# Kernel tuning notes

Measured on AMD Instinct MI355X. Metric: run time of the kernel, lower is better.

The kernel has to match this reference:

```python
import jax, jax.numpy as jnp
import numpy as np

# dims derived from init_kwargs
B, C, T, F = 16, 2, 16, 256
TP, FP = 4, 4            # time/freq patch
MF = F // FP             # 64 freq tokens
TIC = T // TP            # 4 time tokens per chunk
S = MF * TIC             # 256 tokens per chunk
CTX = 3
LEFT = S * CTX           # 768 cached tokens
MT = TIC * (CTX + 1)     # 16 max time positions
D, H, G = 512, 8, 4      # d_model, q heads, kv groups
HD = D // H              # 64
R = H // G               # 2 q-heads per kv group
L = 4                    # layers
FFH = 4 * D
EPS = 1e-5


def _ln(x, g, b):
    m = jnp.mean(x, -1, keepdims=True)
    v = jnp.mean((x - m) ** 2, -1, keepdims=True)
    return (x - m) * jax.lax.rsqrt(v + EPS) * g + b


def setup_inputs() -> dict:
    key = jax.random.key(0)
    ks = iter(jax.random.split(key, 20))
    rn = lambda shape, s=0.05: jax.random.normal(next(ks), shape, jnp.float32) * s
    return {
        "x": rn((B, C, T, F), 1.0),
        "cache_k": rn((L, B, G, LEFT, HD), 1.0),
        "cache_v": rn((L, B, G, LEFT, HD), 1.0),
        "in_W": rn((TP * FP * C, D)), "in_b": jnp.zeros((D,)),
        "ln1_g": jnp.ones((L, D)), "ln1_b": jnp.zeros((L, D)),
        "Wq": rn((L, D, D)), "bq": jnp.zeros((L, D)),
        "Wk": rn((L, D, G * HD)), "bk": jnp.zeros((L, G * HD)),
        "Wv": rn((L, D, G * HD)), "bv": jnp.zeros((L, G * HD)),
        "Wo": rn((L, D, D)), "bo": jnp.zeros((L, D)),
        "rel_time": rn((L, 2 * MT - 1, H)), "rel_freq": rn((L, 2 * MF - 1, H)),
        "res_a": jnp.ones((L,)),
        "ln2_g": jnp.ones((L, D)), "ln2_b": jnp.zeros((L, D)),
        "W1": rn((L, D, FFH)), "b1": jnp.zeros((L, FFH)),
        "W3": rn((L, D, FFH)), "b3": jnp.zeros((L, FFH)),
        "W2": rn((L, FFH, D)), "b2": jnp.zeros((L, D)),
        "res_f": jnp.ones((L,)),
        "out_W": rn((D, TP * FP * C)), "out_b": jnp.zeros((TP * FP * C,)),
    }


def reference(x, cache_k, cache_v, in_W, in_b, ln1_g, ln1_b, Wq, bq, Wk, bk, Wv, bv,
              Wo, bo, rel_time, rel_freq, res_a, ln2_g, ln2_b, W1, b1, W3, b3, W2, b2,
              res_f, out_W, out_b):
    # patchify: (B,C,T,F) -> (B, S, TP*FP*C), token order time-major / freq inner
    h = jnp.transpose(x, (0, 2, 3, 1)).reshape(B, TIC, TP, MF, FP, C)
    h = jnp.transpose(h, (0, 1, 3, 2, 4, 5)).reshape(B, S, TP * FP * C)
    h = h @ in_W + in_b  # (B,S,D)

    # 2D relative position indices (identical each layer)
    K = LEFT + S
    q_idx = jnp.arange(S)
    k_idx = jnp.arange(K)
    qt = LEFT // MF + q_idx // MF  # query time = cache time offset + local time
    qf = q_idx % MF
    kt = k_idx // MF
    kf = k_idx % MF
    dt = qt[:, None] - kt[None, :] + (MT - 1)  # (S,K) in [0, 2*MT-2]
    df = qf[:, None] - kf[None, :] + (MF - 1)  # (S,K) in [0, 2*MF-2]
    scale = 1.0 / np.sqrt(HD).astype(np.float32)

    new_ck, new_cv = [], []
    for l in range(L):
        # --- streaming GQA attention with 2D rel-pos and KV cache ---
        xin = _ln(h, ln1_g[l], ln1_b[l])
        q = (xin @ Wq[l] + bq[l]).reshape(B, S, H, HD)
        k = (xin @ Wk[l] + bk[l]).reshape(B, S, G, HD)
        v = (xin @ Wv[l] + bv[l]).reshape(B, S, G, HD)
        k_full = jnp.concatenate([cache_k[l], jnp.transpose(k, (0, 2, 1, 3))], axis=2)  # (B,G,K,HD)
        v_full = jnp.concatenate([cache_v[l], jnp.transpose(v, (0, 2, 1, 3))], axis=2)
        new_ck.append(k_full[:, :, -LEFT:])
        new_cv.append(v_full[:, :, -LEFT:])
        # group q heads: head h -> group h // R
        scores = jnp.einsum('bsgrd,bgtd->bgrst', q.reshape(B, S, G, R, HD), k_full) * scale
        bias = rel_time[l][dt] + rel_freq[l][df]          # (S,K,H)
        bias = jnp.transpose(bias, (2, 0, 1)).reshape(G, R, S, K)
        attn = jax.nn.softmax(scores + bias[None], axis=-1)
        o = jnp.einsum('bgrst,bgtd->bsgrd', attn, v_full).reshape(B, S, D)
        o = o @ Wo[l] + bo[l]
        h = h + res_a[l] * o  # dropout/droppath identity at eval
        # --- SwiGLU FFN ---
        xin = _ln(h, ln2_g[l], ln2_b[l])
        ff = (jax.nn.silu(xin @ W1[l] + b1[l]) * (xin @ W3[l] + b3[l])) @ W2[l] + b2[l]
        h = h + res_f[l] * ff

    y = h @ out_W + out_b  # (B,S,TP*FP*C)
    # unpatchify back to (B,C,T,F)
    y = y.reshape(B, TIC, MF, TP, FP, C)
    y = jnp.transpose(y, (0, 1, 3, 2, 4, 5)).reshape(B, T, F, C)
    y = jnp.transpose(y, (0, 3, 1, 2))
    return y, jnp.stack(new_ck), jnp.stack(new_cv)
```

## Files before the change

kernel.cpp:

```cpp
#include <hip/hip_runtime.h>
#include <stdint.h>

typedef __attribute__((ext_vector_type(8))) short bf16x8;
typedef __attribute__((ext_vector_type(4))) float f32x4;

#define B_    16
#define S_    256
#define LEFT_ 768
#define KT_   1024
#define D_    512
#define H_    8
#define G_    4
#define HD_   64
#define L_    4
#define FFH_  2048
#define M_    4096

__device__ __forceinline__ unsigned short f2b(float f){
  unsigned u = __float_as_uint(f);
  u += 0x7fffu + ((u>>16)&1u);
  return (unsigned short)(u>>16);
}

__device__ __forceinline__ void gl_lds16(const unsigned short* g, void* l){
  __builtin_amdgcn_global_load_lds(
    (const __attribute__((address_space(1))) unsigned int*)g,
    (__attribute__((address_space(3))) unsigned int*)l, 16, 0, 0);
}

template<int BM, int BN, int WM, int WN, class BRowF>
__device__ __forceinline__ void mfma_core(
    const unsigned short* Abase, int lda, int m0, BRowF brow,
    int kd, char* As, char* Bs, f32x4* acc)
{
  constexpr int FR = WM/16, FC = WN/16;
  constexpr int NWC = BN/WN;
  constexpr int CA = BM/64, CB = BN/64;
  const int tid = threadIdx.x, wave = tid>>6, lane = tid&63;
  const int wr = wave / NWC, wc = wave % NWC;
  const int lr = lane>>2;
  const int swl = (lane&3) ^ ((lane>>2)&3) ^ (lane>>4);

  auto stage = [&](int buf, int k0){
    #pragma unroll
    for (int i = 0; i < CA; ++i) {
      const int chunk = wave*CA + i;
      const unsigned short* gp = Abase + (size_t)(m0 + chunk*16 + lr)*lda + k0 + swl*8;
      gl_lds16(gp, As + buf*(BM*64) + chunk*1024);
    }
    #pragma unroll
    for (int i = 0; i < CB; ++i) {
      const int chunk = wave*CB + i;
      const unsigned short* gp = brow(chunk*16 + lr) + k0 + swl*8;
      gl_lds16(gp, Bs + buf*(BN*64) + chunk*1024);
    }
  };

  stage(0, 0);
  __syncthreads();
  int cur = 0;
  for (int k0 = 0; k0 < kd; k0 += 32) {
    if (k0 + 32 < kd) stage(cur^1, k0 + 32);
    bf16x8 af[FR], bfr[FC];
    #pragma unroll
    for (int r = 0; r < FR; ++r)
      af[r] = *(const bf16x8*)(As + cur*(BM*64) + (wr*WM + r*16 + (lane&15))*64 + swl*16);
    #pragma unroll
    for (int c = 0; c < FC; ++c)
      bfr[c] = *(const bf16x8*)(Bs + cur*(BN*64) + (wc*WN + c*16 + (lane&15))*64 + swl*16);
    #pragma unroll
    for (int r = 0; r < FR; ++r)
      #pragma unroll
      for (int c = 0; c < FC; ++c)
        acc[r*FC+c] = __builtin_amdgcn_mfma_f32_16x16x32_bf16(af[r], bfr[c], acc[r*FC+c], 0, 0, 0);
    __syncthreads();
    cur ^= 1;
  }
}

__global__ __launch_bounds__(256) void transpose_cvt(
    const float* __restrict__ src, unsigned short* __restrict__ dst,
    int K, int N, int ntk, int ntn)
{
  __shared__ float t[64][65];
  int bx = blockIdx.x;
  int kt = bx % ntk; int nt = (bx/ntk) % ntn; int l = bx/(ntk*ntn);
  src += (size_t)l*K*N; dst += (size_t)l*N*K;
  const int k0 = kt*64, n0 = nt*64;
  const int tid = threadIdx.x;
  #pragma unroll
  for (int i = 0; i < 4; ++i) {
    int kr = (tid>>4) + i*16;
    const float4 v = *(const float4*)&src[(size_t)(k0+kr)*N + n0 + (tid&15)*4];
    t[kr][(tid&15)*4+0]=v.x; t[kr][(tid&15)*4+1]=v.y;
    t[kr][(tid&15)*4+2]=v.z; t[kr][(tid&15)*4+3]=v.w;
  }
  __syncthreads();
  const int nn = tid>>2, kk = (tid&3)*16;
  unsigned w[8];
  #pragma unroll
  for (int j = 0; j < 8; ++j)
    w[j] = (unsigned)f2b(t[kk+2*j][nn]) | ((unsigned)f2b(t[kk+2*j+1][nn])<<16);
  size_t off = (size_t)(n0+nn)*K + k0 + kk;
  *(uint4*)&dst[off]     = make_uint4(w[0],w[1],w[2],w[3]);
  *(uint4*)&dst[off + 8] = make_uint4(w[4],w[5],w[6],w[7]);
}

__global__ __launch_bounds__(256) void patchify_inproj(
    const float* __restrict__ x, const float* __restrict__ inW,
    const float* __restrict__ inb, float* __restrict__ h)
{
  int bs = blockIdx.x;
  int b = bs >> 8, s = bs & 255;
  int tic = s >> 6, mf = s & 63;
  __shared__ float ps[32];
  int tid = threadIdx.x;
  if (tid < 32) {
    int tp = tid >> 3, fp = (tid >> 1) & 3, c = tid & 1;
    ps[tid] = x[((size_t)(b*2 + c)*16 + tic*4 + tp)*256 + mf*4 + fp];
  }
  __syncthreads();
  #pragma unroll
  for (int rep = 0; rep < 2; ++rep) {
    int d = tid + rep*256;
    float acc = inb[d];
    #pragma unroll
    for (int i = 0; i < 32; ++i) acc += ps[i] * inW[i*D_ + d];
    h[(size_t)bs*D_ + d] = acc;
  }
}

__global__ __launch_bounds__(256) void ln_kernel(
    const float* __restrict__ in, unsigned short* __restrict__ out,
    const float* __restrict__ g, const float* __restrict__ bta)
{
  size_t row = blockIdx.x;
  const float* rp = in + row*D_;
  int tid = threadIdx.x;
  float x0 = rp[tid], x1 = rp[tid+256];
  float s = x0 + x1, sq = x0*x0 + x1*x1;
  __shared__ float red[10];
  #pragma unroll
  for (int o = 32; o > 0; o >>= 1) {
    s  += __shfl_down(s,  o, 64);
    sq += __shfl_down(sq, o, 64);
  }
  if ((tid & 63) == 0) { red[tid>>6] = s; red[4 + (tid>>6)] = sq; }
  __syncthreads();
  if (tid == 0) {
    float ts = red[0]+red[1]+red[2]+red[3];
    float tq = red[4]+red[5]+red[6]+red[7];
    float mean = ts * (1.0f/D_);
    float var  = tq * (1.0f/D_) - mean*mean;
    red[8] = mean; red[9] = 1.0f / sqrtf(var + 1e-5f);
  }
  __syncthreads();
  float mean = red[8], inv = red[9];
  unsigned short* op = out + row*D_;
  op[tid]     = f2b((x0-mean)*inv*g[tid]     + bta[tid]);
  op[tid+256] = f2b((x1-mean)*inv*g[tid+256] + bta[tid+256]);
}

__global__ __launch_bounds__(256) void qkv_gemm(
    const unsigned short* __restrict__ xin,
    const unsigned short* __restrict__ Wqt, const unsigned short* __restrict__ Wkt,
    const unsigned short* __restrict__ Wvt,
    const float* __restrict__ bq, const float* __restrict__ bk_, const float* __restrict__ bv_,
    unsigned short* __restrict__ q_bf, unsigned short* __restrict__ kf_bf,
    unsigned short* __restrict__ vt_bf, float* __restrict__ nck, float* __restrict__ ncv)
{
  __shared__ alignas(16) char As[2*128*64];
  __shared__ alignas(16) char Bs[2*128*64];
  f32x4 acc[16] = {};
  const int bx = blockIdx.x;
  const int mt = bx >> 3, nt = bx & 7;
  const int m0 = mt*128, n0 = nt*128;
  auto brow = [&](int r) -> const unsigned short* {
    int n = n0 + r;
    return n < 512 ? Wqt + (size_t)n*512
         : n < 768 ? Wkt + (size_t)(n-512)*512
                   : Wvt + (size_t)(n-768)*512;
  };
  mfma_core<128,128,64,64>(xin, 512, m0, brow, 512, As, Bs, acc);
  const int lane = threadIdx.x & 63, wave = threadIdx.x >> 6;
  const int wr = wave >> 1, wc = wave & 1;
  #pragma unroll
  for (int r = 0; r < 4; ++r)
  #pragma unroll
  for (int c = 0; c < 4; ++c) {
    f32x4 v = acc[r*4+c];
    #pragma unroll
    for (int reg = 0; reg < 4; ++reg) {
      int m = m0 + wr*64 + r*16 + ((lane>>4)<<2) + reg;
      int n = n0 + wc*64 + c*16 + (lane&15);
      float val = v[reg];
      int b = m >> 8, s = m & 255;
      if (n < 512) {
        q_bf[(size_t)m*512 + n] = f2b(val + bq[n]);
      } else if (n < 768) {
        int g = (n-512) >> 6, hd = n & 63;
        float kv = val + bk_[n-512];
        kf_bf[((size_t)(b*4+g)*1024 + 768 + s)*64 + hd] = f2b(kv);
        nck [((size_t)(b*4+g)*768  + 512 + s)*64 + hd] = kv;
      } else {
        int g = (n-768) >> 6, hd = n & 63;
        float vv = val + bv_[n-768];
        vt_bf[((size_t)(b*4+g)*64 + hd)*1024 + 768 + s] = f2b(vv);
        ncv  [((size_t)(b*4+g)*768 + 512 + s)*64 + hd] = vv;
      }
    }
  }
}

__global__ __launch_bounds__(256) void merge_k(
    const float* __restrict__ ck, unsigned short* __restrict__ kf_bf,
    float* __restrict__ nck)
{
  size_t idx = (size_t)blockIdx.x*256 + threadIdx.x;
  int hd4 = idx & 15;
  size_t t  = (idx >> 4) % 768;
  size_t bg = idx / (16*768);
  const float4 v = ((const float4*)ck)[idx];
  uint2 pk;
  pk.x = (unsigned)f2b(v.x) | ((unsigned)f2b(v.y)<<16);
  pk.y = (unsigned)f2b(v.z) | ((unsigned)f2b(v.w)<<16);
  *(uint2*)&kf_bf[((bg*1024 + t)*64) + hd4*4] = pk;
  if (t >= 256)
    ((float4*)nck)[(bg*768 + (t-256))*16 + hd4] = v;
}

__global__ __launch_bounds__(256) void merge_vt(
    const float* __restrict__ cv, unsigned short* __restrict__ vt_bf,
    float* __restrict__ ncv)
{
  __shared__ float t[64][65];
  const int bg = blockIdx.x / 12, tt = blockIdx.x % 12;
  const int t0 = tt*64;
  const int tid = threadIdx.x;
  #pragma unroll
  for (int i = 0; i < 4; ++i) {
    int tr = (tid>>4) + i*16;
    const float4 v = ((const float4*)cv)[((size_t)bg*768 + t0+tr)*16 + (tid&15)];
    t[tr][(tid&15)*4+0]=v.x; t[tr][(tid&15)*4+1]=v.y;
    t[tr][(tid&15)*4+2]=v.z; t[tr][(tid&15)*4+3]=v.w;
    if (t0+tr >= 256)
      ((float4*)ncv)[((size_t)bg*768 + t0+tr-256)*16 + (tid&15)] = v;
  }
  __syncthreads();
  const int hd = tid>>2, tc = (tid&3)*16;
  unsigned w[8];
  #pragma unroll
  for (int j = 0; j < 8; ++j)
    w[j] = (unsigned)f2b(t[tc+2*j][hd]) | ((unsigned)f2b(t[tc+2*j+1][hd])<<16);
  size_t off = ((size_t)bg*64 + hd)*1024 + t0 + tc;
  *(uint4*)&vt_bf[off]     = make_uint4(w[0],w[1],w[2],w[3]);
  *(uint4*)&vt_bf[off + 8] = make_uint4(w[4],w[5],w[6],w[7]);
}

__global__ __launch_bounds__(256) void flash_attn(
    const unsigned short* __restrict__ q_bf,
    const unsigned short* __restrict__ kf_bf,
    const unsigned short* __restrict__ vt_bf,
    const float* __restrict__ relt,
    const float* __restrict__ relf,
    unsigned short* __restrict__ att_bf)
{
  const int bx = blockIdx.x;
  const int qt = bx & 3, hh = (bx>>2) & 7, b = bx >> 5;
  const int g = hh >> 1;
  const int tid = threadIdx.x, wave = tid>>6, lane = tid&63;
  const int lg = lane>>4, lq = lane&15;
  const int q0 = qt*64;

  __shared__ alignas(16) char Ks[2][8192];
  __shared__ alignas(16) char Vs[2][8192];

  const unsigned short* kfb  = kf_bf + (size_t)(b*4+g)*1024*64;
  const unsigned short* vtb2 = vt_bf + (size_t)(b*4+g)*64*1024;

  auto stage = [&](int buf, int t){
    #pragma unroll
    for (int it = 0; it < 2; ++it) {
      int slot = it*256 + tid;
      int r = slot>>3, p = slot&7, u = p ^ (r&7);
      gl_lds16(kfb + (size_t)(t*64 + r)*64 + u*8, Ks[buf] + slot*16);
      gl_lds16(vtb2 + (size_t)r*1024 + t*64 + u*8, Vs[buf] + slot*16);
    }
  };

  const unsigned short* qrow = q_bf + ((size_t)(b*256 + q0 + wave*16 + lq))*512 + hh*64;
  bf16x8 qfrag[2];
  qfrag[0] = *(const bf16x8*)(qrow + lg*8);
  qfrag[1] = *(const bf16x8*)(qrow + 32 + lg*8);

  float bias_f[4][4];
  {
    int sq = wave*16 + lq;
    #pragma unroll
    for (int f = 0; f < 4; ++f)
      #pragma unroll
      for (int r = 0; r < 4; ++r)
        bias_f[f][r] = relf[((sq - (f*16 + lg*4 + r)) + 63)*8 + hh];
  }

  f32x4 ot[4] = {};
  float m_run = -1e30f, l_part = 0.f;

  stage(0, 0);
  __syncthreads();

  for (int t = 0; t < 16; ++t) {
    const int cur = t & 1;
    if (t + 1 < 16) stage(cur^1, t+1);

    f32x4 st[4] = {};
    #pragma unroll
    for (int c = 0; c < 2; ++c)
      #pragma unroll
      for (int f = 0; f < 4; ++f) {
        int row = f*16 + lq;
        int pu = (c*4 + lg) ^ (row & 7);
        bf16x8 kf_ = *(const bf16x8*)(Ks[cur] + row*128 + pu*16);
        st[f] = __builtin_amdgcn_mfma_f32_16x16x32_bf16(kf_, qfrag[c], st[f], 0,0,0);
      }

    const float bias_t = relt[(27 + qt - t)*8 + hh];
    float mt = -1e30f;
    #pragma unroll
    for (int f = 0; f < 4; ++f)
      #pragma unroll
      for (int r = 0; r < 4; ++r) {
        float v = st[f][r]*0.125f + bias_t + bias_f[f][r];
        st[f][r] = v;
        mt = fmaxf(mt, v);
      }
    mt = fmaxf(mt, __shfl_xor(mt, 16, 64));
    mt = fmaxf(mt, __shfl_xor(mt, 32, 64));
    const float m_new = fmaxf(m_run, mt);
    const float corr = __expf(m_run - m_new);
    m_run = m_new;
    l_part *= corr;
    #pragma unroll
    for (int f = 0; f < 4; ++f) {
      ot[f][0] *= corr; ot[f][1] *= corr; ot[f][2] *= corr; ot[f][3] *= corr;
    }
    float psum = 0.f;
    unsigned r01[4], r23[4];
    #pragma unroll
    for (int f = 0; f < 4; ++f) {
      float e0 = __expf(st[f][0] - m_new);
      float e1 = __expf(st[f][1] - m_new);
      float e2 = __expf(st[f][2] - m_new);
      float e3 = __expf(st[f][3] - m_new);
      psum += (e0+e1)+(e2+e3);
      r01[f] = (unsigned)f2b(e0) | ((unsigned)f2b(e1)<<16);
      r23[f] = (unsigned)f2b(e2) | ((unsigned)f2b(e3)<<16);
    }
    l_part += psum;

    const int src0 = (lg&1)*32 + lq;
    const int src1 = src0 + 16;
    const bool hi = (lg>>1) != 0;
    #pragma unroll
    for (int c = 0; c < 2; ++c) {
      unsigned a0 = (unsigned)__shfl((int)r01[c*2],   src0, 64);
      unsigned b0 = (unsigned)__shfl((int)r01[c*2+1], src0, 64);
      unsigned a1 = (unsigned)__shfl((int)r23[c*2],   src0, 64);
      unsigned b1 = (unsigned)__shfl((int)r23[c*2+1], src0, 64);
      unsigned a2 = (unsigned)__shfl((int)r01[c*2],   src1, 64);
      unsigned b2 = (unsigned)__shfl((int)r01[c*2+1], src1, 64);
      unsigned a3 = (unsigned)__shfl((int)r23[c*2],   src1, 64);
      unsigned b3 = (unsigned)__shfl((int)r23[c*2+1], src1, 64);
      uint4 bw;
      bw.x = hi ? b0 : a0;
      bw.y = hi ? b1 : a1;
      bw.z = hi ? b2 : a2;
      bw.w = hi ? b3 : a3;
      bf16x8 pfrag = *(bf16x8*)&bw;
      #pragma unroll
      for (int f = 0; f < 4; ++f) {
        int row = f*16 + lq;
        int pu = (c*4 + lg) ^ (row & 7);
        bf16x8 vf_ = *(const bf16x8*)(Vs[cur] + row*128 + pu*16);
        ot[f] = __builtin_amdgcn_mfma_f32_16x16x32_bf16(vf_, pfrag, ot[f], 0,0,0);
      }
    }
    __syncthreads();
  }

  float l_tot = l_part + __shfl_xor(l_part, 16, 64);
  l_tot += __shfl_xor(l_tot, 32, 64);
  const float inv = 1.0f / l_tot;
  unsigned short* orow = att_bf + ((size_t)(b*256 + q0 + wave*16 + lq))*512 + hh*64;
  #pragma unroll
  for (int f = 0; f < 4; ++f) {
    uint2 w;
    w.x = (unsigned)f2b(ot[f][0]*inv) | ((unsigned)f2b(ot[f][1]*inv)<<16);
    w.y = (unsigned)f2b(ot[f][2]*inv) | ((unsigned)f2b(ot[f][3]*inv)<<16);
    *(uint2*)(orow + f*16 + lg*4) = w;
  }
}

__global__ __launch_bounds__(256) void ffn1_gemm(
    const unsigned short* __restrict__ xin,
    const unsigned short* __restrict__ W1t, const unsigned short* __restrict__ W3t,
    const float* __restrict__ b1_, const float* __restrict__ b3_,
    unsigned short* __restrict__ ff_bf)
{
  __shared__ alignas(16) char As[2*128*64];
  __shared__ alignas(16) char Bs[2*128*64];
  f32x4 acc[16] = {};
  const int bx = blockIdx.x;
  const int nt = bx & 31, mt = bx >> 5;
  const int m0 = mt*128, n0 = nt*128;
  auto brow = [&](int r) -> const unsigned short* {
    int p = n0 + r;
    int pb = p >> 4;
    int j = ((pb>>1)<<4) | (p & 15);
    return (pb & 1) ? W3t + (size_t)j*512 : W1t + (size_t)j*512;
  };
  mfma_core<128,128,64,64>(xin, 512, m0, brow, 512, As, Bs, acc);
  const int lane = threadIdx.x & 63, wave = threadIdx.x >> 6;
  const int wr = wave >> 1, wc = wave & 1;
  #pragma unroll
  for (int r = 0; r < 4; ++r)
  #pragma unroll
  for (int cp = 0; cp < 4; cp += 2) {
    f32x4 va = acc[r*4+cp];
    f32x4 vb = acc[r*4+cp+1];
    #pragma unroll
    for (int reg = 0; reg < 4; ++reg) {
      int m = m0 + wr*64 + r*16 + ((lane>>4)<<2) + reg;
      int p = n0 + wc*64 + cp*16 + (lane&15);
      int j = ((p>>5)<<4) | (p & 15);
      float a = va[reg] + b1_[j];
      float bb = vb[reg] + b3_[j];
      float gval = (a / (1.0f + __expf(-a))) * bb;
      ff_bf[(size_t)m*2048 + j] = f2b(gval);
    }
  }
}

__global__ __launch_bounds__(256) void res_gemm(
    const unsigned short* __restrict__ A, int lda,
    const unsigned short* __restrict__ Wt, int kd,
    const float* __restrict__ bias, const float* __restrict__ resv,
    float* __restrict__ h)
{
  __shared__ alignas(16) char As[2*64*64];
  __shared__ alignas(16) char Bs[2*128*64];
  f32x4 acc[8] = {};
  const int bx = blockIdx.x;
  const int mt = bx >> 2, nt = bx & 3;
  const int m0 = mt*64, n0 = nt*128;
  auto brow = [&](int r) -> const unsigned short* {
    return Wt + (size_t)(n0 + r)*kd;
  };
  mfma_core<64,128,32,64>(A, lda, m0, brow, kd, As, Bs, acc);
  const float rv = resv[0];
  const int lane = threadIdx.x & 63, wave = threadIdx.x >> 6;
  const int wr = wave >> 1, wc = wave & 1;
  #pragma unroll
  for (int r = 0; r < 2; ++r)
  #pragma unroll
  for (int c = 0; c < 4; ++c) {
    f32x4 v = acc[r*4+c];
    #pragma unroll
    for (int reg = 0; reg < 4; ++reg) {
      int m = m0 + wr*32 + r*16 + ((lane>>4)<<2) + reg;
      int n = n0 + wc*64 + c*16 + (lane&15);
      h[(size_t)m*512 + n] += rv * (v[reg] + bias[n]);
    }
  }
}

__global__ __launch_bounds__(256) void outproj_kernel(
    const float* __restrict__ h, const float* __restrict__ outW,
    const float* __restrict__ outb, float* __restrict__ y)
{
  int bs = blockIdx.x;
  int b = bs >> 8, s = bs & 255;
  int tic = s >> 6, mf = s & 63;
  __shared__ float hr[512];
  __shared__ float part[8][32];
  int tid = threadIdx.x;
  hr[tid]     = h[(size_t)bs*D_ + tid];
  hr[tid+256] = h[(size_t)bs*D_ + tid + 256];
  __syncthreads();
  int i = tid & 31, seg = tid >> 5;
  float acc = 0.0f;
  #pragma unroll
  for (int k = 0; k < 64; ++k) acc += hr[seg*64 + k] * outW[(seg*64 + k)*32 + i];
  part[seg][i] = acc;
  __syncthreads();
  if (tid < 32) {
    float v = outb[tid];
    #pragma unroll
    for (int s2 = 0; s2 < 8; ++s2) v += part[s2][tid];
    int tp = tid >> 3, fp = (tid >> 1) & 3, c = tid & 1;
    y[((size_t)(b*2 + c)*16 + tic*4 + tp)*256 + mf*4 + fp] = v;
  }
}

extern "C" void kernel_launch(void* const* d_in, const int* in_sizes, int n_in,
                              void* d_out, int out_size, void* d_ws, size_t ws_size,
                              hipStream_t stream) {
  (void)in_sizes; (void)n_in; (void)out_size; (void)ws_size;
  const float* x        = (const float*)d_in[0];
  const float* cache_k  = (const float*)d_in[1];
  const float* cache_v  = (const float*)d_in[2];
  const float* in_W     = (const float*)d_in[3];
  const float* in_b     = (const float*)d_in[4];
  const float* ln1_g    = (const float*)d_in[5];
  const float* ln1_b    = (const float*)d_in[6];
  const float* Wq       = (const float*)d_in[7];
  const float* bq       = (const float*)d_in[8];
  const float* Wk       = (const float*)d_in[9];
  const float* bk       = (const float*)d_in[10];
  const float* Wv       = (const float*)d_in[11];
  const float* bv       = (const float*)d_in[12];
  const float* Wo       = (const float*)d_in[13];
  const float* bo       = (const float*)d_in[14];
  const float* rel_time = (const float*)d_in[15];
  const float* rel_freq = (const float*)d_in[16];
  const float* res_a    = (const float*)d_in[17];
  const float* ln2_g    = (const float*)d_in[18];
  const float* ln2_b    = (const float*)d_in[19];
  const float* W1       = (const float*)d_in[20];
  const float* b1       = (const float*)d_in[21];
  const float* W3       = (const float*)d_in[22];
  const float* b3       = (const float*)d_in[23];
  const float* W2       = (const float*)d_in[24];
  const float* b2       = (const float*)d_in[25];
  const float* res_f    = (const float*)d_in[26];
  const float* out_W    = (const float*)d_in[27];
  const float* out_b    = (const float*)d_in[28];

  char* ws = (char*)d_ws;
  size_t o = 0;
  float* h            = (float*)(ws + o);          o += (size_t)4096*512*4;
  unsigned short* xin = (unsigned short*)(ws + o); o += (size_t)4096*512*2;
  unsigned short* qb  = (unsigned short*)(ws + o); o += (size_t)4096*512*2;
  unsigned short* att = (unsigned short*)(ws + o); o += (size_t)4096*512*2;
  unsigned short* kfb = (unsigned short*)(ws + o); o += (size_t)64*1024*64*2;
  unsigned short* vtb = (unsigned short*)(ws + o); o += (size_t)64*64*1024*2;
  unsigned short* Wqt = (unsigned short*)(ws + o); o += (size_t)4*512*512*2;
  unsigned short* Wkt = (unsigned short*)(ws + o); o += (size_t)4*256*512*2;
  unsigned short* Wvt = (unsigned short*)(ws + o); o += (size_t)4*256*512*2;
  unsigned short* Wot = (unsigned short*)(ws + o); o += (size_t)4*512*512*2;
  unsigned short* W1t = (unsigned short*)(ws + o); o += (size_t)4*2048*512*2;
  unsigned short* W3t = (unsigned short*)(ws + o); o += (size_t)4*2048*512*2;
  unsigned short* W2t = (unsigned short*)(ws + o); o += (size_t)4*512*2048*2;
  unsigned short* ffb = (unsigned short*)(ws + o);

  float* y    = (float*)d_out;
  float* nck0 = y + 131072;
  float* ncv0 = nck0 + 12582912;

  transpose_cvt<<<256,  256, 0, stream>>>(Wq, Wqt, 512, 512, 8, 8);
  transpose_cvt<<<128,  256, 0, stream>>>(Wk, Wkt, 512, 256, 8, 4);
  transpose_cvt<<<128,  256, 0, stream>>>(Wv, Wvt, 512, 256, 8, 4);
  transpose_cvt<<<256,  256, 0, stream>>>(Wo, Wot, 512, 512, 8, 8);
  transpose_cvt<<<1024, 256, 0, stream>>>(W1, W1t, 512, 2048, 8, 32);
  transpose_cvt<<<1024, 256, 0, stream>>>(W3, W3t, 512, 2048, 8, 32);
  transpose_cvt<<<1024, 256, 0, stream>>>(W2, W2t, 2048, 512, 32, 8);

  patchify_inproj<<<M_, 256, 0, stream>>>(x, in_W, in_b, h);

  for (int l = 0; l < L_; ++l) {
    ln_kernel<<<M_, 256, 0, stream>>>(h, xin, ln1_g + l*512, ln1_b + l*512);
    qkv_gemm<<<256, 256, 0, stream>>>(
        xin, Wqt + (size_t)l*512*512, Wkt + (size_t)l*256*512, Wvt + (size_t)l*256*512,
        bq + l*512, bk + l*256, bv + l*256,
        qb, kfb, vtb, nck0 + (size_t)l*3145728, ncv0 + (size_t)l*3145728);
    merge_k <<<3072, 256, 0, stream>>>(cache_k + (size_t)l*3145728, kfb,
                                       nck0 + (size_t)l*3145728);
    merge_vt<<<768, 256, 0, stream>>>(cache_v + (size_t)l*3145728, vtb,
                                      ncv0 + (size_t)l*3145728);
    flash_attn<<<512, 256, 0, stream>>>(qb, kfb, vtb,
        rel_time + l*31*8, rel_freq + l*127*8, att);
    res_gemm<<<256, 256, 0, stream>>>(att, 512, Wot + (size_t)l*512*512, 512,
                                      bo + l*512, res_a + l, h);
    ln_kernel<<<M_, 256, 0, stream>>>(h, xin, ln2_g + l*512, ln2_b + l*512);
    ffn1_gemm<<<1024, 256, 0, stream>>>(
        xin, W1t + (size_t)l*2048*512, W3t + (size_t)l*2048*512,
        b1 + l*2048, b3 + l*2048, ffb);
    res_gemm<<<256, 256, 0, stream>>>(ffb, 2048, W2t + (size_t)l*512*2048, 2048,
                                      b2 + l*512, res_f + l, h);
  }

  outproj_kernel<<<M_, 256, 0, stream>>>(h, out_W, out_b, y);
}
```

Baseline: 712.5 us.

## Fuse LayerNorm into QKV GEMM and merge transpose and KV-cache launches

Folds the pre-attention LayerNorm into the QKV GEMM. Each block computes the row statistics from the fp32 residual stream and normalises and converts A tiles to bf16 on the fly, using a smaller 64x128 tile and twice as many blocks. The seven weight-transpose launches are combined into one kernel, and the K and V cache merge kernels into one. This removes the xin round trip and several launches per layer, but every N-tile block recomputes the LN statistics (eight times per row) and the A loads become fp32 reads with more ALU work in the GEMM loop.

```diff
diff --git a/kernel.cpp b/kernel.cpp
--- a/kernel.cpp
+++ b/kernel.cpp
@@ -78,12 +78,11 @@
   }
 }
 
-__global__ __launch_bounds__(256) void transpose_cvt(
+__device__ __forceinline__ void tcvt_body(
     const float* __restrict__ src, unsigned short* __restrict__ dst,
-    int K, int N, int ntk, int ntn)
+    int K, int N, int ntk, int ntn, int bx)
 {
   __shared__ float t[64][65];
-  int bx = blockIdx.x;
   int kt = bx % ntk; int nt = (bx/ntk) % ntn; int l = bx/(ntk*ntn);
   src += (size_t)l*K*N; dst += (size_t)l*N*K;
   const int k0 = kt*64, n0 = nt*64;
@@ -104,6 +103,26 @@
   size_t off = (size_t)(n0+nn)*K + k0 + kk;
   *(uint4*)&dst[off]     = make_uint4(w[0],w[1],w[2],w[3]);
   *(uint4*)&dst[off + 8] = make_uint4(w[4],w[5],w[6],w[7]);
+}
+
+__global__ __launch_bounds__(256) void transpose_all(
+    const float* __restrict__ Wq, const float* __restrict__ Wk,
+    const float* __restrict__ Wv, const float* __restrict__ Wo,
+    const float* __restrict__ W1, const float* __restrict__ W3,
+    const float* __restrict__ W2,
+    unsigned short* __restrict__ Wqt, unsigned short* __restrict__ Wkt,
+    unsigned short* __restrict__ Wvt, unsigned short* __restrict__ Wot,
+    unsigned short* __restrict__ W1t, unsigned short* __restrict__ W3t,
+    unsigned short* __restrict__ W2t)
+{
+  int bx = blockIdx.x;
+  if      (bx < 256)  tcvt_body(Wq, Wqt, 512, 512, 8, 8,  bx);
+  else if (bx < 384)  tcvt_body(Wk, Wkt, 512, 256, 8, 4,  bx-256);
+  else if (bx < 512)  tcvt_body(Wv, Wvt, 512, 256, 8, 4,  bx-384);
+  else if (bx < 768)  tcvt_body(Wo, Wot, 512, 512, 8, 8,  bx-512);
+  else if (bx < 1792) tcvt_body(W1, W1t, 512, 2048, 8, 32, bx-768);
+  else if (bx < 2816) tcvt_body(W3, W3t, 512, 2048, 8, 32, bx-1792);
+  else                tcvt_body(W2, W2t, 2048, 512, 32, 8, bx-2816);
 }
 
 __global__ __launch_bounds__(256) void patchify_inproj(
@@ -161,37 +180,123 @@
   op[tid+256] = f2b((x1-mean)*inv*g[tid+256] + bta[tid+256]);
 }
 
-__global__ __launch_bounds__(256) void qkv_gemm(
-    const unsigned short* __restrict__ xin,
+__global__ __launch_bounds__(256) void qkv_ln_gemm(
+    const float* __restrict__ h,
+    const float* __restrict__ lng, const float* __restrict__ lnb,
     const unsigned short* __restrict__ Wqt, const unsigned short* __restrict__ Wkt,
     const unsigned short* __restrict__ Wvt,
     const float* __restrict__ bq, const float* __restrict__ bk_, const float* __restrict__ bv_,
     unsigned short* __restrict__ q_bf, unsigned short* __restrict__ kf_bf,
     unsigned short* __restrict__ vt_bf, float* __restrict__ nck, float* __restrict__ ncv)
 {
-  __shared__ alignas(16) char As[2*128*64];
-  __shared__ alignas(16) char Bs[2*128*64];
-  f32x4 acc[16] = {};
+  __shared__ alignas(16) char As[2][64*64];
+  __shared__ alignas(16) char Bs[2][128*64];
+  __shared__ float sm[64], sr[64];
   const int bx = blockIdx.x;
   const int mt = bx >> 3, nt = bx & 7;
-  const int m0 = mt*128, n0 = nt*128;
-  auto brow = [&](int r) -> const unsigned short* {
-    int n = n0 + r;
+  const int m0 = mt*64, n0 = nt*128;
+  const int tid = threadIdx.x, wave = tid>>6, lane = tid&63;
+
+  {
+    const int r = tid >> 2, qd = tid & 3;
+    const float* rp = h + (size_t)(m0 + r)*512 + qd*128;
+    float s = 0.f, sq = 0.f;
+    #pragma unroll
+    for (int i = 0; i < 32; ++i) {
+      float4 v = ((const float4*)rp)[i];
+      s  += (v.x+v.y)+(v.z+v.w);
+      sq += (v.x*v.x+v.y*v.y)+(v.z*v.z+v.w*v.w);
+    }
+    s += __shfl_xor(s,1,64); sq += __shfl_xor(sq,1,64);
+    s += __shfl_xor(s,2,64); sq += __shfl_xor(sq,2,64);
+    if (qd == 0) {
+      float mean = s*(1.f/512.f);
+      sm[r] = mean;
+      sr[r] = rsqrtf(sq*(1.f/512.f) - mean*mean + 1e-5f);
+    }
+  }
+
+  const int ar = tid >> 2, au = tid & 3;
+  const int ap = au ^ (ar&3) ^ ((ar>>2)&3);
+  const float* arow = h + (size_t)(m0 + ar)*512;
+
+  const int lr = lane>>2;
+  const int swl = (lane&3) ^ ((lane>>2)&3) ^ (lane>>4);
+  auto brow = [&](int rr) -> const unsigned short* {
+    int n = n0 + rr;
     return n < 512 ? Wqt + (size_t)n*512
          : n < 768 ? Wkt + (size_t)(n-512)*512
                    : Wvt + (size_t)(n-768)*512;
   };
-  mfma_core<128,128,64,64>(xin, 512, m0, brow, 512, As, Bs, acc);
-  const int lane = threadIdx.x & 63, wave = threadIdx.x >> 6;
+  auto stageB = [&](int buf, int k0){
+    #pragma unroll
+    for (int i = 0; i < 2; ++i) {
+      const int chunk = wave*2 + i;
+      gl_lds16(brow(chunk*16+lr) + k0 + swl*8, (char*)Bs[buf] + chunk*1024);
+    }
+  };
+
+  __syncthreads();
+  const float mean_r = sm[ar], rstd_r = sr[ar];
+
+  float4 av[6];
+  auto loadA = [&](int k0){
+    av[0] = *(const float4*)(arow + k0 + au*8);
+    av[1] = *(const float4*)(arow + k0 + au*8 + 4);
+    av[2] = *(const float4*)(lng  + k0 + au*8);
+    av[3] = *(const float4*)(lng  + k0 + au*8 + 4);
+    av[4] = *(const float4*)(lnb  + k0 + au*8);
+    av[5] = *(const float4*)(lnb  + k0 + au*8 + 4);
+  };
+  auto writeA = [&](int buf){
+    const float* xv = (const float*)&av[0];
+    const float* gv = (const float*)&av[2];
+    const float* bv2 = (const float*)&av[4];
+    unsigned w[4];
+    #pragma unroll
+    for (int j = 0; j < 4; ++j) {
+      float e0 = (xv[2*j]   - mean_r)*rstd_r*gv[2*j]   + bv2[2*j];
+      float e1 = (xv[2*j+1] - mean_r)*rstd_r*gv[2*j+1] + bv2[2*j+1];
+      w[j] = (unsigned)f2b(e0) | ((unsigned)f2b(e1)<<16);
+    }
+    *(uint4*)((char*)As[buf] + ar*64 + ap*16) = make_uint4(w[0],w[1],w[2],w[3]);
+  };
+
+  loadA(0);
+  stageB(0, 0);
+  writeA(0);
+  __syncthreads();
+
+  f32x4 acc[8] = {};
   const int wr = wave >> 1, wc = wave & 1;
-  #pragma unroll
-  for (int r = 0; r < 4; ++r)
+  for (int k0 = 0; k0 < 512; k0 += 32) {
+    const int cur = (k0>>5)&1;
+    const bool more = (k0 + 32 < 512);
+    if (more) { stageB(cur^1, k0+32); loadA(k0+32); }
+    bf16x8 af[2], bfv[4];
+    #pragma unroll
+    for (int r = 0; r < 2; ++r)
+      af[r] = *(const bf16x8*)((char*)As[cur] + (wr*32 + r*16 + (lane&15))*64 + swl*16);
+    #pragma unroll
+    for (int c = 0; c < 4; ++c)
+      bfv[c] = *(const bf16x8*)((char*)Bs[cur] + (wc*64 + c*16 + (lane&15))*64 + swl*16);
+    #pragma unroll
+    for (int r = 0; r < 2; ++r)
+      #pragma unroll
+      for (int c = 0; c < 4; ++c)
+        acc[r*4+c] = __builtin_amdgcn_mfma_f32_16x16x32_bf16(af[r], bfv[c], acc[r*4+c], 0,0,0);
+    if (more) writeA(cur^1);
+    __syncthreads();
+  }
+
+  #pragma unroll
+  for (int r = 0; r < 2; ++r)
   #pragma unroll
   for (int c = 0; c < 4; ++c) {
     f32x4 v = acc[r*4+c];
     #pragma unroll
     for (int reg = 0; reg < 4; ++reg) {
-      int m = m0 + wr*64 + r*16 + ((lane>>4)<<2) + reg;
+      int m = m0 + wr*32 + r*16 + ((lane>>4)<<2) + reg;
       int n = n0 + wc*64 + c*16 + (lane&15);
       float val = v[reg];
       int b = m >> 8, s = m & 255;
@@ -212,49 +317,49 @@
   }
 }
 
-__global__ __launch_bounds__(256) void merge_k(
-    const float* __restrict__ ck, unsigned short* __restrict__ kf_bf,
-    float* __restrict__ nck)
-{
-  size_t idx = (size_t)blockIdx.x*256 + threadIdx.x;
-  int hd4 = idx & 15;
-  size_t t  = (idx >> 4) % 768;
-  size_t bg = idx / (16*768);
-  const float4 v = ((const float4*)ck)[idx];
-  uint2 pk;
-  pk.x = (unsigned)f2b(v.x) | ((unsigned)f2b(v.y)<<16);
-  pk.y = (unsigned)f2b(v.z) | ((unsigned)f2b(v.w)<<16);
-  *(uint2*)&kf_bf[((bg*1024 + t)*64) + hd4*4] = pk;
-  if (t >= 256)
-    ((float4*)nck)[(bg*768 + (t-256))*16 + hd4] = v;
-}
-
-__global__ __launch_bounds__(256) void merge_vt(
-    const float* __restrict__ cv, unsigned short* __restrict__ vt_bf,
-    float* __restrict__ ncv)
+__global__ __launch_bounds__(256) void merge_kv(
+    const float* __restrict__ ck, const float* __restrict__ cv,
+    unsigned short* __restrict__ kf_bf, unsigned short* __restrict__ vt_bf,
+    float* __restrict__ nck, float* __restrict__ ncv)
 {
   __shared__ float t[64][65];
-  const int bg = blockIdx.x / 12, tt = blockIdx.x % 12;
-  const int t0 = tt*64;
+  const int bb = blockIdx.x;
   const int tid = threadIdx.x;
-  #pragma unroll
-  for (int i = 0; i < 4; ++i) {
-    int tr = (tid>>4) + i*16;
-    const float4 v = ((const float4*)cv)[((size_t)bg*768 + t0+tr)*16 + (tid&15)];
-    t[tr][(tid&15)*4+0]=v.x; t[tr][(tid&15)*4+1]=v.y;
-    t[tr][(tid&15)*4+2]=v.z; t[tr][(tid&15)*4+3]=v.w;
-    if (t0+tr >= 256)
-      ((float4*)ncv)[((size_t)bg*768 + t0+tr-256)*16 + (tid&15)] = v;
-  }
-  __syncthreads();
-  const int hd = tid>>2, tc = (tid&3)*16;
-  unsigned w[8];
-  #pragma unroll
-  for (int j = 0; j < 8; ++j)
-    w[j] = (unsigned)f2b(t[tc+2*j][hd]) | ((unsigned)f2b(t[tc+2*j+1][hd])<<16);
-  size_t off = ((size_t)bg*64 + hd)*1024 + t0 + tc;
-  *(uint4*)&vt_bf[off]     = make_uint4(w[0],w[1],w[2],w[3]);
-  *(uint4*)&vt_bf[off + 8] = make_uint4(w[4],w[5],w[6],w[7]);
+  if (bb < 3072) {
+    size_t idx = (size_t)bb*256 + tid;
+    int hd4 = idx & 15;
+    size_t tt = (idx >> 4) % 768;
+    size_t bg = idx / (16*768);
+    const float4 v = ((const float4*)ck)[idx];
+    uint2 pk;
+    pk.x = (unsigned)f2b(v.x) | ((unsigned)f2b(v.y)<<16);
+    pk.y = (unsigned)f2b(v.z) | ((unsigned)f2b(v.w)<<16);
+    *(uint2*)&kf_bf[((bg*1024 + tt)*64) + hd4*4] = pk;
+    if (tt >= 256)
+      ((float4*)nck)[(bg*768 + (tt-256))*16 + hd4] = v;
+  } else {
+    const int bi = bb - 3072;
+    const int bg = bi / 12, tt = bi % 12;
+    const int t0 = tt*64;
+    #pragma unroll
+    for (int i = 0; i < 4; ++i) {
+      int tr = (tid>>4) + i*16;
+      const float4 v = ((const float4*)cv)[((size_t)bg*768 + t0+tr)*16 + (tid&15)];
+      t[tr][(tid&15)*4+0]=v.x; t[tr][(tid&15)*4+1]=v.y;
+      t[tr][(tid&15)*4+2]=v.z; t[tr][(tid&15)*4+3]=v.w;
+      if (t0+tr >= 256)
+        ((float4*)ncv)[((size_t)bg*768 + t0+tr-256)*16 + (tid&15)] = v;
+    }
+    __syncthreads();
+    const int hd = tid>>2, tc = (tid&3)*16;
+    unsigned w[8];
+    #pragma unroll
+    for (int j = 0; j < 8; ++j)
+      w[j] = (unsigned)f2b(t[tc+2*j][hd]) | ((unsigned)f2b(t[tc+2*j+1][hd])<<16);
+    size_t off = ((size_t)bg*64 + hd)*1024 + t0 + tc;
+    *(uint4*)&vt_bf[off]     = make_uint4(w[0],w[1],w[2],w[3]);
+    *(uint4*)&vt_bf[off + 8] = make_uint4(w[4],w[5],w[6],w[7]);
+  }
 }
 
 __global__ __launch_bounds__(256) void flash_attn(
@@ -557,26 +662,20 @@
   float* nck0 = y + 131072;
   float* ncv0 = nck0 + 12582912;
 
-  transpose_cvt<<<256,  256, 0, stream>>>(Wq, Wqt, 512, 512, 8, 8);
-  transpose_cvt<<<128,  256, 0, stream>>>(Wk, Wkt, 512, 256, 8, 4);
-  transpose_cvt<<<128,  256, 0, stream>>>(Wv, Wvt, 512, 256, 8, 4);
-  transpose_cvt<<<256,  256, 0, stream>>>(Wo, Wot, 512, 512, 8, 8);
-  transpose_cvt<<<1024, 256, 0, stream>>>(W1, W1t, 512, 2048, 8, 32);
-  transpose_cvt<<<1024, 256, 0, stream>>>(W3, W3t, 512, 2048, 8, 32);
-  transpose_cvt<<<1024, 256, 0, stream>>>(W2, W2t, 2048, 512, 32, 8);
+  transpose_all<<<3840, 256, 0, stream>>>(Wq, Wk, Wv, Wo, W1, W3, W2,
+                                          Wqt, Wkt, Wvt, Wot, W1t, W3t, W2t);
 
   patchify_inproj<<<M_, 256, 0, stream>>>(x, in_W, in_b, h);
 
   for (int l = 0; l < L_; ++l) {
-    ln_kernel<<<M_, 256, 0, stream>>>(h, xin, ln1_g + l*512, ln1_b + l*512);
-    qkv_gemm<<<256, 256, 0, stream>>>(
-        xin, Wqt + (size_t)l*512*512, Wkt + (size_t)l*256*512, Wvt + (size_t)l*256*512,
+    qkv_ln_gemm<<<512, 256, 0, stream>>>(
+        h, ln1_g + l*512, ln1_b + l*512,
+        Wqt + (size_t)l*512*512, Wkt + (size_t)l*256*512, Wvt + (size_t)l*256*512,
         bq + l*512, bk + l*256, bv + l*256,
         qb, kfb, vtb, nck0 + (size_t)l*3145728, ncv0 + (size_t)l*3145728);
-    merge_k <<<3072, 256, 0, stream>>>(cache_k + (size_t)l*3145728, kfb,
-                                       nck0 + (size_t)l*3145728);
-    merge_vt<<<768, 256, 0, stream>>>(cache_v + (size_t)l*3145728, vtb,
-                                      ncv0 + (size_t)l*3145728);
+    merge_kv<<<3840, 256, 0, stream>>>(
+        cache_k + (size_t)l*3145728, cache_v + (size_t)l*3145728,
+        kfb, vtb, nck0 + (size_t)l*3145728, ncv0 + (size_t)l*3145728);
     flash_attn<<<512, 256, 0, stream>>>(qb, kfb, vtb,
         rel_time + l*31*8, rel_freq + l*127*8, att);
     res_gemm<<<256, 256, 0, stream>>>(att, 512, Wot + (size_t)l*512*512, 512,
```

Result: no change. 710.1 us (-0.3%).
